# Performance work log

Hardware: AMD Instinct MI355X
Metric: run time of the kernel (lower is better)

## Reference

```python
import jax
import jax.numpy as jnp
from jax import lax
import numpy as np

# module hyperparameters (match init_kwargs)
IN_C, OUT_C = 32, 64
K, STRIDE, PAD, DIL = 3, 1, 1, 1
GRID_SIZE, ORDER = 5, 3
GRID_LO, GRID_HI = -1.0, 1.0
SCALE_SPLINE = 1.0
EPS = 1e-8


def _knot_grid():
    # grid = arange(-order, grid_size+order+1) * h + lo ; length = grid_size + 2*order + 1 = 12
    h = (GRID_HI - GRID_LO) / GRID_SIZE
    return jnp.arange(-ORDER, GRID_SIZE + ORDER + 1, dtype=jnp.float32) * h + GRID_LO


def _bspline_bases(x):
    """Cox-de Boor recursion. x: (N, P) -> bases: (N, P, GRID_SIZE+ORDER)."""
    grid = _knot_grid()
    xe = x[..., None]  # (N, P, 1)
    bases = ((xe >= grid[:-1]) & (xe < grid[1:])).astype(x.dtype)  # (N, P, 11)
    for k in range(1, ORDER + 1):
        left_den = jnp.maximum(grid[k:-1] - grid[:-(k + 1)], EPS)
        right_den = jnp.maximum(grid[k + 1:] - grid[1:-k], EPS)
        bases = ((xe - grid[:-(k + 1)]) / left_den * bases[..., :-1]
                 + (grid[k + 1:] - xe) / right_den * bases[..., 1:])
    return bases  # (N, P, 8)


def setup_inputs() -> dict:
    key = jax.random.key(0)
    k1, k2, k3 = jax.random.split(key, 3)
    x = jax.random.normal(k1, (4, IN_C, 56, 56), dtype=jnp.float32)
    base_weight = jax.random.normal(k2, (OUT_C, IN_C, K, K), dtype=jnp.float32) * 0.05
    spline_weight = jax.random.normal(k3, (OUT_C, IN_C * K * K, GRID_SIZE + ORDER), dtype=jnp.float32) * 0.05
    spline_scaler = jnp.ones((OUT_C,), dtype=jnp.float32)
    return {"x": x, "base_weight": base_weight,
            "spline_weight": spline_weight, "spline_scaler": spline_scaler}


def reference(x, base_weight, spline_weight, spline_scaler):
    B, C, H, W = x.shape
    pad = [(PAD, PAD), (PAD, PAD)]
    # base path: conv2d -> SiLU
    base_conv = lax.conv_general_dilated(
        x, base_weight, window_strides=(STRIDE, STRIDE), padding=pad,
        rhs_dilation=(DIL, DIL), dimension_numbers=("NCHW", "OIHW", "NCHW"))
    base_out = jax.nn.silu(base_conv)

    # unfold: (B, C*K*K, oh, ow) with torch Unfold channel ordering (c, kh, kw)
    patches = lax.conv_general_dilated_patches(
        x, filter_shape=(K, K), window_strides=(STRIDE, STRIDE), padding=pad,
        rhs_dilation=(DIL, DIL))
    oh, ow = patches.shape[2], patches.shape[3]
    num_patches = oh * ow
    # (B*num_patches, C*K*K)
    pf = patches.reshape(B, C * K * K, num_patches).transpose(0, 2, 1).reshape(-1, C * K * K)

    bases = _bspline_bases(pf)  # (N, P, F)
    # contract patch-dim and basis-dim against spline weights
    spl = jnp.einsum("npf,opf->no", bases, spline_weight) * spline_scaler  # (N, O)
    spl = spl.reshape(B, num_patches, OUT_C).transpose(0, 2, 1).reshape(B, OUT_C, oh, ow)
    return base_out + SCALE_SPLINE * spl
```

## Files before the change

kernel.cpp:

```cpp
#include <hip/hip_runtime.h>
#include <math.h>


typedef __attribute__((ext_vector_type(8))) short bf16x8;
typedef __attribute__((ext_vector_type(4))) float f32x4;

#define MFMA16(a, b, c) __builtin_amdgcn_mfma_f32_16x16x32_bf16((a), (b), (c), 0, 0, 0)

__device__ __forceinline__ unsigned short f2bf(float f) {
    unsigned u = __builtin_bit_cast(unsigned, f);
    u = (u + 0x7fffu + ((u >> 16) & 1u)) >> 16;
    return (unsigned short)u;
}

__device__ __forceinline__ void eval_bases(float v, float bs[8]) {
    #pragma unroll
    for (int i = 0; i < 8; ++i) bs[i] = 0.0f;
    float t = (v + 2.2f) * 2.5f;
    if (t >= 0.0f && t < 11.0f) {
        int j = (int)t;
        if (j > 10) j = 10;
        float knot = (float)(j - 3) * 0.4f - 1.0f;
        float u  = (v - knot) * 2.5f;
        float um = 1.0f - u;
        float u2 = u * u, u3 = u2 * u;
        const float s6 = 1.0f / 6.0f;
        float w0 = um * um * um * s6;
        float w1 = (3.0f * u3 - 6.0f * u2 + 4.0f) * s6;
        float w2 = (-3.0f * u3 + 3.0f * u2 + 3.0f * u + 1.0f) * s6;
        float w3 = u3 * s6;
        int i0 = j - 3;
        if (i0 >= 0)               bs[i0]     = w0;
        if (i0 + 1 >= 0 && i0 < 7) bs[i0 + 1] = w1;
        if (i0 + 2 >= 0 && i0 < 6) bs[i0 + 2] = w2;
        if (i0 + 3 <= 7)           bs[i0 + 3] = w3;
    }
}

__global__ __launch_bounds__(256)
void cvt_swz_kernel(const float* __restrict__ ws, const float* __restrict__ wb,
                    unsigned short* __restrict__ wst, unsigned short* __restrict__ wbt) {
    int i = blockIdx.x * 256 + threadIdx.x;
    if (i < 147456) {
        int j = i & 7, l = (i >> 3) & 63, t = i >> 9;
        int S = t % 72, nq = t / 72;
        int oc = nq * 16 + (l & 15);
        int k  = S * 32 + (l >> 4) * 8 + j;
        wst[i] = f2bf(ws[oc * 2304 + k]);
    } else {
        int i2 = i - 147456;
        if (i2 < 18432) {
            int j = i2 & 7, l = (i2 >> 3) & 63, t = i2 >> 9;
            int s = t % 9, nq = t / 9;
            int oc = nq * 16 + (l & 15);
            int k  = s * 32 + (l >> 4) * 8 + j;
            wbt[i2] = f2bf(wb[oc * 288 + k]);
        }
    }
}

__global__ __launch_bounds__(512)
void kan_mfma_kernel(const float* __restrict__ x,
                     const float* __restrict__ sc,
                     const unsigned short* __restrict__ wst,
                     const unsigned short* __restrict__ wbt,
                     float* __restrict__ out) {
    __shared__ unsigned short smem[24832];
    unsigned short* sb    = smem;
    unsigned short* patch = smem + 15360;

    const int tid = threadIdx.x;
    const int bx  = blockIdx.x;
    const int b   = bx / 98;
    const int r   = bx - b * 98;
    const int ty  = r / 7;
    const int tx  = r - ty * 7;
    const int h0  = ty * 4, w0 = tx * 8;

    const int lane = tid & 63;
    const int wv   = tid >> 6;
    const int nq   = wv & 3;
    const int mh   = wv >> 2;
    const int ml   = lane & 15;
    const int kg   = lane >> 4;
    const int m    = mh * 16 + ml;
    const int py0  = m >> 3, px0 = m & 7;

    float vv[4];
    #pragma unroll
    for (int j = 0; j < 4; ++j) {
        int i = tid + j * 512;
        float val = 0.0f;
        if (i < 1920) {
            int c  = i / 60;
            int hp = i - c * 60;
            int hy = hp / 10;
            int hx = hp - hy * 10;
            int hh = h0 + hy - 1, ww = w0 + hx - 1;
            if ((unsigned)hh < 56u && (unsigned)ww < 56u)
                val = x[((b * 32 + c) * 56 + hh) * 56 + ww];
        }
        vv[j] = val;
    }
    #pragma unroll
    for (int j = 0; j < 4; ++j) {
        int i = tid + j * 512;
        if (i < 1920) {
            int c  = i / 60;
            int hp = i - c * 60;
            int hy = hp / 10;
            int hx = hp - hy * 10;
            float bs[8];
            eval_bases(vv[j], bs);
            bf16x8 pk;
            #pragma unroll
            for (int j2 = 0; j2 < 8; ++j2) pk[j2] = (short)f2bf(bs[j2]);
            *reinterpret_cast<bf16x8*>(&sb[i * 8]) = pk;
            unsigned short xb = f2bf(vv[j]);
            #pragma unroll
            for (int kh = 0; kh < 3; ++kh) {
                int py = hy - kh;
                if ((unsigned)py < 4u) {
                    #pragma unroll
                    for (int kw = 0; kw < 3; ++kw) {
                        int px = hx - kw;
                        if ((unsigned)px < 8u)
                            patch[(py * 8 + px) * 296 + c * 9 + kh * 3 + kw] = xb;
                    }
                }
            }
        }
    }
    __syncthreads();

    int aoff[9];
    #pragma unroll
    for (int u = 0; u < 9; ++u) {
        int tt  = 4 * u + kg;
        int dc  = tt / 9;
        int tap = tt - dc * 9;
        int kh  = tap / 3;
        int kw  = tap - kh * 3;
        aoff[u] = (dc * 60 + (py0 + kh) * 10 + (px0 + kw)) * 8;
    }

    f32x4 accS = {0.f, 0.f, 0.f, 0.f};
    f32x4 accB = {0.f, 0.f, 0.f, 0.f};

    const unsigned short* bp = wst + (nq * 72 * 64 + lane) * 8;
    int cbase = 0;
    for (int g = 0; g < 8; ++g) {
        #pragma unroll
        for (int u = 0; u < 9; ++u) {
            bf16x8 a  = *reinterpret_cast<const bf16x8*>(&sb[cbase + aoff[u]]);
            bf16x8 bw = *reinterpret_cast<const bf16x8*>(bp + (g * 9 + u) * 512);
            accS = MFMA16(a, bw, accS);
        }
        cbase += 1920;
    }

    {
        const unsigned short* ap  = patch + m * 296 + kg * 8;
        const unsigned short* bbp = wbt + (nq * 9 * 64 + lane) * 8;
        #pragma unroll
        for (int s = 0; s < 9; ++s) {
            bf16x8 a  = *reinterpret_cast<const bf16x8*>(ap + s * 32);
            bf16x8 bw = *reinterpret_cast<const bf16x8*>(bbp + s * 512);
            accB = MFMA16(a, bw, accB);
        }
    }

    const int oc  = nq * 16 + ml;
    const float scv = sc[oc];
    const int rowb = mh * 16 + kg * 4;
    const int py   = rowb >> 3;
    const int pxb  = rowb & 7;
    float* ob = out + ((b * 64 + oc) * 56 + h0 + py) * 56 + w0 + pxb;
    f32x4 res;
    #pragma unroll
    for (int reg = 0; reg < 4; ++reg) {
        float bv = accB[reg];
        float si = bv / (1.0f + __expf(-bv));
        res[reg] = si + scv * accS[reg];
    }
    *reinterpret_cast<f32x4*>(ob) = res;
}

extern "C" void kernel_launch(void* const* d_in, const int* in_sizes, int n_in,
                              void* d_out, int out_size, void* d_ws, size_t ws_size,
                              hipStream_t stream) {
    const float* x  = (const float*)d_in[0];
    const float* wb = (const float*)d_in[1];
    const float* ws = (const float*)d_in[2];
    const float* sc = (const float*)d_in[3];
    float* out = (float*)d_out;

    unsigned short* wst = (unsigned short*)d_ws;
    unsigned short* wbt = wst + 147456;

    cvt_swz_kernel<<<648, 256, 0, stream>>>(ws, wb, wst, wbt);
    kan_mfma_kernel<<<392, 512, 0, stream>>>(x, sc, wst, wbt, out);
}
```

Baseline: 78.27 us.

## Enlarge spatial tile to 8x8 and compute two output-channel tiles per wave

```diff
diff --git a/kernel.cpp b/kernel.cpp
--- a/kernel.cpp
+++ b/kernel.cpp
@@ -53,8 +53,8 @@
             int j = i2 & 7, l = (i2 >> 3) & 63, t = i2 >> 9;
             int s = t % 9, nq = t / 9;
             int oc = nq * 16 + (l & 15);
-            int k  = s * 32 + (l >> 4) * 8 + j;
-            wbt[i2] = f2bf(wb[oc * 288 + k]);
+            int c  = (l >> 4) * 8 + j;
+            wbt[i2] = f2bf(wb[oc * 288 + c * 9 + s]);
         }
     }
 }
@@ -65,35 +65,35 @@
                      const unsigned short* __restrict__ wst,
                      const unsigned short* __restrict__ wbt,
                      float* __restrict__ out) {
-    __shared__ unsigned short smem[24832];
-    unsigned short* sb    = smem;
-    unsigned short* patch = smem + 15360;
+    __shared__ unsigned short smem[29600];
+    unsigned short* sb = smem;
+    unsigned short* sx = smem + 25600;
 
     const int tid = threadIdx.x;
     const int bx  = blockIdx.x;
-    const int b   = bx / 98;
-    const int r   = bx - b * 98;
+    const int b   = bx / 49;
+    const int r   = bx - b * 49;
     const int ty  = r / 7;
     const int tx  = r - ty * 7;
-    const int h0  = ty * 4, w0 = tx * 8;
+    const int h0  = ty * 8, w0 = tx * 8;
 
     const int lane = tid & 63;
     const int wv   = tid >> 6;
-    const int nq   = wv & 3;
-    const int mh   = wv >> 2;
+    const int mh   = wv & 3;
+    const int nh   = wv >> 2;
     const int ml   = lane & 15;
     const int kg   = lane >> 4;
-    const int m    = mh * 16 + ml;
-    const int py0  = m >> 3, px0 = m & 7;
-
-    float vv[4];
-    #pragma unroll
-    for (int j = 0; j < 4; ++j) {
+    const int p    = mh * 16 + ml;
+    const int py0  = p >> 3, px0 = p & 7;
+
+    float vv[7];
+    #pragma unroll
+    for (int j = 0; j < 7; ++j) {
         int i = tid + j * 512;
         float val = 0.0f;
-        if (i < 1920) {
-            int c  = i / 60;
-            int hp = i - c * 60;
+        if (i < 3200) {
+            int c  = i / 100;
+            int hp = i - c * 100;
             int hy = hp / 10;
             int hx = hp - hy * 10;
             int hh = h0 + hy - 1, ww = w0 + hx - 1;
@@ -103,32 +103,18 @@
         vv[j] = val;
     }
     #pragma unroll
-    for (int j = 0; j < 4; ++j) {
+    for (int j = 0; j < 7; ++j) {
         int i = tid + j * 512;
-        if (i < 1920) {
-            int c  = i / 60;
-            int hp = i - c * 60;
-            int hy = hp / 10;
-            int hx = hp - hy * 10;
+        if (i < 3200) {
+            int c  = i / 100;
+            int hp = i - c * 100;
             float bs[8];
             eval_bases(vv[j], bs);
             bf16x8 pk;
             #pragma unroll
             for (int j2 = 0; j2 < 8; ++j2) pk[j2] = (short)f2bf(bs[j2]);
             *reinterpret_cast<bf16x8*>(&sb[i * 8]) = pk;
-            unsigned short xb = f2bf(vv[j]);
-            #pragma unroll
-            for (int kh = 0; kh < 3; ++kh) {
-                int py = hy - kh;
-                if ((unsigned)py < 4u) {
-                    #pragma unroll
-                    for (int kw = 0; kw < 3; ++kw) {
-                        int px = hx - kw;
-                        if ((unsigned)px < 8u)
-                            patch[(py * 8 + px) * 296 + c * 9 + kh * 3 + kw] = xb;
-                    }
-                }
-            }
+            sx[hp * 40 + c] = f2bf(vv[j]);
         }
     }
     __syncthreads();
@@ -141,49 +127,60 @@
         int tap = tt - dc * 9;
         int kh  = tap / 3;
         int kw  = tap - kh * 3;
-        aoff[u] = (dc * 60 + (py0 + kh) * 10 + (px0 + kw)) * 8;
-    }
-
-    f32x4 accS = {0.f, 0.f, 0.f, 0.f};
-    f32x4 accB = {0.f, 0.f, 0.f, 0.f};
-
-    const unsigned short* bp = wst + (nq * 72 * 64 + lane) * 8;
+        aoff[u] = (dc * 100 + (py0 + kh) * 10 + (px0 + kw)) * 8;
+    }
+
+    f32x4 accS0 = {0.f,0.f,0.f,0.f}, accS1 = {0.f,0.f,0.f,0.f};
+    f32x4 accB0 = {0.f,0.f,0.f,0.f}, accB1 = {0.f,0.f,0.f,0.f};
+
+    const unsigned short* bp0 = wst + (nh * 2) * 72 * 512 + lane * 8;
+    const unsigned short* bp1 = bp0 + 72 * 512;
     int cbase = 0;
     for (int g = 0; g < 8; ++g) {
         #pragma unroll
         for (int u = 0; u < 9; ++u) {
-            bf16x8 a  = *reinterpret_cast<const bf16x8*>(&sb[cbase + aoff[u]]);
-            bf16x8 bw = *reinterpret_cast<const bf16x8*>(bp + (g * 9 + u) * 512);
-            accS = MFMA16(a, bw, accS);
-        }
-        cbase += 1920;
+            bf16x8 a   = *reinterpret_cast<const bf16x8*>(&sb[cbase + aoff[u]]);
+            bf16x8 bw0 = *reinterpret_cast<const bf16x8*>(bp0 + (g * 9 + u) * 512);
+            bf16x8 bw1 = *reinterpret_cast<const bf16x8*>(bp1 + (g * 9 + u) * 512);
+            accS0 = MFMA16(a, bw0, accS0);
+            accS1 = MFMA16(a, bw1, accS1);
+        }
+        cbase += 3200;
     }
 
     {
-        const unsigned short* ap  = patch + m * 296 + kg * 8;
-        const unsigned short* bbp = wbt + (nq * 9 * 64 + lane) * 8;
+        const unsigned short* bbp0 = wbt + (nh * 2) * 9 * 512 + lane * 8;
+        const unsigned short* bbp1 = bbp0 + 9 * 512;
         #pragma unroll
         for (int s = 0; s < 9; ++s) {
-            bf16x8 a  = *reinterpret_cast<const bf16x8*>(ap + s * 32);
-            bf16x8 bw = *reinterpret_cast<const bf16x8*>(bbp + s * 512);
-            accB = MFMA16(a, bw, accB);
-        }
-    }
-
-    const int oc  = nq * 16 + ml;
-    const float scv = sc[oc];
-    const int rowb = mh * 16 + kg * 4;
-    const int py   = rowb >> 3;
-    const int pxb  = rowb & 7;
-    float* ob = out + ((b * 64 + oc) * 56 + h0 + py) * 56 + w0 + pxb;
-    f32x4 res;
-    #pragma unroll
-    for (int reg = 0; reg < 4; ++reg) {
-        float bv = accB[reg];
-        float si = bv / (1.0f + __expf(-bv));
-        res[reg] = si + scv * accS[reg];
-    }
-    *reinterpret_cast<f32x4*>(ob) = res;
+            int kh = s / 3, kw = s - kh * 3;
+            int cell = (py0 + kh) * 10 + (px0 + kw);
+            bf16x8 a   = *reinterpret_cast<const bf16x8*>(&sx[cell * 40 + kg * 8]);
+            bf16x8 bw0 = *reinterpret_cast<const bf16x8*>(bbp0 + s * 512);
+            bf16x8 bw1 = *reinterpret_cast<const bf16x8*>(bbp1 + s * 512);
+            accB0 = MFMA16(a, bw0, accB0);
+            accB1 = MFMA16(a, bw1, accB1);
+        }
+    }
+
+    const int py  = mh * 2 + (kg >> 1);
+    const int pxb = (kg & 1) * 4;
+    #pragma unroll
+    for (int t16 = 0; t16 < 2; ++t16) {
+        const int oc = nh * 32 + t16 * 16 + ml;
+        const float scv = sc[oc];
+        const f32x4 aS = t16 ? accS1 : accS0;
+        const f32x4 aB = t16 ? accB1 : accB0;
+        f32x4 res;
+        #pragma unroll
+        for (int reg = 0; reg < 4; ++reg) {
+            float bv = aB[reg];
+            float si = bv / (1.0f + __expf(-bv));
+            res[reg] = si + scv * aS[reg];
+        }
+        float* ob = out + ((b * 64 + oc) * 56 + h0 + py) * 56 + w0 + pxb;
+        *reinterpret_cast<f32x4*>(ob) = res;
+    }
 }
 
 extern "C" void kernel_launch(void* const* d_in, const int* in_sizes, int n_in,
@@ -199,5 +196,5 @@
     unsigned short* wbt = wst + 147456;
 
     cvt_swz_kernel<<<648, 256, 0, stream>>>(ws, wb, wst, wbt);
-    kan_mfma_kernel<<<392, 512, 0, stream>>>(x, sc, wst, wbt, out);
-}
+    kan_mfma_kernel<<<196, 512, 0, stream>>>(x, sc, wst, wbt, out);
+}
```

Result: no change. 79.59 us (+1.7%).
